# Performance work log

Hardware: AMD Instinct MI355X
Metric: run time of the kernel (lower is better)

The kernel has to match this reference:

```python
import jax, jax.numpy as jnp
import numpy as np

B, T, M = 32, 1024, 40
CD, H, C = 128, 256, 10  # conv_dims, rnn_hidden_dims, num_classes
DN = ('NCHW', 'OIHW', 'NCHW')


def _conv_block(x, W, b, pool):
    # 3x3 'same' conv + ReLU + max-pool (1, pool) over the mel axis
    y = jax.lax.conv_general_dilated(x, W, (1, 1), 'SAME', dimension_numbers=DN)
    y = jax.nn.relu(y + b[None, :, None, None])
    return jax.lax.reduce_window(y, -jnp.inf, jax.lax.max,
                                 (1, 1, 1, pool), (1, 1, 1, pool), 'VALID')


def setup_inputs() -> dict:
    key = jax.random.key(0)
    ks = jax.random.split(key, 12)
    inp = {}
    inp['x'] = jax.random.normal(ks[0], (B, 1, T, M), dtype=jnp.float32)
    inp['targets'] = (jax.random.uniform(ks[1], (B, T, C)) > 0.5).astype(jnp.float32)
    inp['force_mask'] = jax.random.randint(ks[2], (T, B), 0, 2, dtype=jnp.int32)
    s = 0.05
    inp['W1'] = jax.random.normal(ks[3], (CD, 1, 3, 3), dtype=jnp.float32) * s
    inp['b1'] = jnp.zeros((CD,), jnp.float32)
    inp['W2'] = jax.random.normal(ks[4], (CD, CD, 3, 3), dtype=jnp.float32) * s
    inp['b2'] = jnp.zeros((CD,), jnp.float32)
    inp['W3'] = jax.random.normal(ks[5], (CD, CD, 3, 3), dtype=jnp.float32) * s
    inp['b3'] = jnp.zeros((CD,), jnp.float32)
    inp['W_ih'] = jax.random.normal(ks[6], (3 * H, CD + C), dtype=jnp.float32) * s
    inp['W_hh'] = jax.random.normal(ks[7], (3 * H, H), dtype=jnp.float32) * s
    inp['b_ih'] = jnp.zeros((3 * H,), jnp.float32)
    inp['b_hh'] = jnp.zeros((3 * H,), jnp.float32)
    inp['Wf'] = jax.random.normal(ks[8], (C, H), dtype=jnp.float32) * s
    inp['bf'] = jnp.zeros((C,), jnp.float32)
    return inp


def reference(x, targets, force_mask, W1, b1, W2, b2, W3, b3,
              W_ih, W_hh, b_ih, b_hh, Wf, bf):
    # CNN feature extractor: mel axis 40 -> 8 -> 2 -> 1
    f = _conv_block(x, W1, b1, 5)
    f = _conv_block(f, W2, b2, 4)
    f = _conv_block(f, W3, b3, 2)          # [B, CD, T, 1]
    feats = f[..., 0].transpose(2, 0, 1)    # [T, B, CD]
    tgt_t = targets.transpose(1, 0, 2)       # [T, B, C]

    def step(carry, inp_t):
        h, tf = carry
        xt, tg, fm = inp_t                  # [B,CD], [B,C], [B]
        xc = jnp.concatenate([xt, tf], axis=-1)
        gi = xc @ W_ih.T + b_ih
        gh = h @ W_hh.T + b_hh
        i_r, i_z, i_n = jnp.split(gi, 3, axis=-1)
        h_r, h_z, h_n = jnp.split(gh, 3, axis=-1)
        r = jax.nn.sigmoid(i_r + h_r)
        z = jax.nn.sigmoid(i_z + h_z)
        n = jnp.tanh(i_n + r * h_n)
        h_new = (1.0 - z) * n + z * h
        out = h_new @ Wf.T + bf             # [B, C]
        pred = (jax.nn.sigmoid(out) > 0.5).astype(out.dtype)
        tf_new = jnp.where(fm[:, None] > 0, tg, pred)
        return (h_new, tf_new), out

    h0 = jnp.zeros((B, H), x.dtype)
    tf0 = jnp.zeros((B, C), x.dtype)
    _, outs = jax.lax.scan(step, (h0, tf0), (feats, tgt_t, force_mask))
    return outs.transpose(1, 0, 2)          # [B, T, C]
```

## Files before the change

kernel.cpp:

```cpp
#include <hip/hip_runtime.h>
#include <math.h>

#define B_ 32
#define T_ 1024
#define M_ 40

__global__ void prep_kernel(const float* __restrict__ W_hh, const float* __restrict__ W2,
                            const float* __restrict__ W3, const float* __restrict__ W_ih,
                            float* __restrict__ WhhT, float* __restrict__ W2t,
                            float* __restrict__ W3t, float* __restrict__ WihT4) {
  int idx = blockIdx.x * 256 + threadIdx.x;
  if (idx < 196608) {
    int k = idx / 768, j = idx % 768;
    WhhT[idx] = W_hh[j * 256 + k];
    return;
  }
  idx -= 196608;
  if (idx < 147456) {
    int tap = idx >> 14, ci = (idx >> 7) & 127, co = idx & 127;
    W2t[idx] = W2[(co * 128 + ci) * 9 + tap];
    return;
  }
  idx -= 147456;
  if (idx < 147456) {
    int tap = idx >> 14, ci = (idx >> 7) & 127, co = idx & 127;
    W3t[idx] = W3[(co * 128 + ci) * 9 + tap];
    return;
  }
  idx -= 147456;
  if (idx < 98304) {
    int khi = idx / 3072, rem = idx % 3072, j = rem >> 2, klo = rem & 3;
    WihT4[idx] = W_ih[j * 138 + khi * 4 + klo];
  }
}

__global__ __launch_bounds__(256) void conv12_kernel(
    const float* __restrict__ x, const float* __restrict__ W1, const float* __restrict__ b1,
    const float* __restrict__ W2t, const float* __restrict__ b2, float* __restrict__ y2) {
  __shared__ float xt[8 * 42];
  __shared__ float y1s[6 * 128 * 12];
  const int tid = threadIdx.x;
  const int t0 = blockIdx.x * 4;
  const int b = blockIdx.y;
  for (int idx = tid; idx < 8 * 42; idx += 256) {
    int row = idx / 42, slot = idx % 42;
    int t_in = t0 - 2 + row, m = slot - 1;
    float v = 0.f;
    if (t_in >= 0 && t_in < T_ && m >= 0 && m < M_) v = x[(b * T_ + t_in) * M_ + m];
    xt[idx] = v;
  }
  __syncthreads();
  const int c = tid & 127, q = tid >> 7;
  float w1[9];
#pragma unroll
  for (int i = 0; i < 9; ++i) w1[i] = W1[c * 9 + i];
  const float b1c = b1[c];
  for (int rr = 0; rr < 3; ++rr) {
    const int r = q * 3 + rr;
    const int t_in = t0 - 1 + r;
    float* yrow = &y1s[(r * 128 + c) * 12];
    if (t_in < 0 || t_in >= T_) {
#pragma unroll
      for (int s = 0; s < 12; ++s) yrow[s] = 0.f;
    } else {
      yrow[0] = 0.f; yrow[9] = 0.f; yrow[10] = 0.f; yrow[11] = 0.f;
#pragma unroll
      for (int mo = 0; mo < 8; ++mo) {
        float mx = -1e30f;
#pragma unroll
        for (int i5 = 0; i5 < 5; ++i5) {
          const int mp = mo * 5 + i5;
          float s = b1c;
#pragma unroll
          for (int dt = 0; dt < 3; ++dt)
#pragma unroll
            for (int dm = 0; dm < 3; ++dm)
              s += xt[(r + dt) * 42 + mp + dm] * w1[dt * 3 + dm];
          mx = fmaxf(mx, s);
        }
        yrow[1 + mo] = fmaxf(mx, 0.f);
      }
    }
  }
  __syncthreads();
  const int co = c, tq = q;
  float acc[2][8];
#pragma unroll
  for (int tl = 0; tl < 2; ++tl)
#pragma unroll
    for (int mo = 0; mo < 8; ++mo) acc[tl][mo] = 0.f;
  for (int ci = 0; ci < 128; ++ci) {
    float w[9];
#pragma unroll
    for (int i = 0; i < 9; ++i) w[i] = W2t[i * 16384 + ci * 128 + co];
    float xv[4][10];
#pragma unroll
    for (int rr = 0; rr < 4; ++rr) {
      const float* p = &y1s[((2 * tq + rr) * 128 + ci) * 12];
      const float4 a = *(const float4*)p;
      const float4 bq = *(const float4*)(p + 4);
      const float2 cq = *(const float2*)(p + 8);
      xv[rr][0] = a.x; xv[rr][1] = a.y; xv[rr][2] = a.z; xv[rr][3] = a.w;
      xv[rr][4] = bq.x; xv[rr][5] = bq.y; xv[rr][6] = bq.z; xv[rr][7] = bq.w;
      xv[rr][8] = cq.x; xv[rr][9] = cq.y;
    }
#pragma unroll
    for (int dt = 0; dt < 3; ++dt)
#pragma unroll
      for (int dm = 0; dm < 3; ++dm) {
        const float wv = w[dt * 3 + dm];
#pragma unroll
        for (int tl = 0; tl < 2; ++tl)
#pragma unroll
          for (int mo = 0; mo < 8; ++mo)
            acc[tl][mo] += xv[tl + dt][mo + dm] * wv;
      }
  }
  const float b2c = b2[co];
#pragma unroll
  for (int tl = 0; tl < 2; ++tl) {
    const int t = t0 + 2 * tq + tl;
    float m0 = fmaxf(fmaxf(acc[tl][0], acc[tl][1]), fmaxf(acc[tl][2], acc[tl][3])) + b2c;
    float m1 = fmaxf(fmaxf(acc[tl][4], acc[tl][5]), fmaxf(acc[tl][6], acc[tl][7])) + b2c;
    y2[((b * T_ + t) * 2 + 0) * 128 + co] = fmaxf(m0, 0.f);
    y2[((b * T_ + t) * 2 + 1) * 128 + co] = fmaxf(m1, 0.f);
  }
}

__global__ __launch_bounds__(256) void conv3_kernel(
    const float* __restrict__ y2, const float* __restrict__ W3t, const float* __restrict__ b3,
    float* __restrict__ feats) {
  __shared__ float y2s[6 * 128 * 4];
  const int tid = threadIdx.x;
  const int t0 = blockIdx.x * 4;
  const int b = blockIdx.y;
  for (int idx = tid; idx < 768; idx += 256) {
    int row = idx / 128, ci = idx % 128;
    y2s[(row * 128 + ci) * 4 + 0] = 0.f;
    y2s[(row * 128 + ci) * 4 + 3] = 0.f;
  }
  for (int idx = tid; idx < 6 * 256; idx += 256) {
    int row = idx / 256, rem = idx % 256;
    int m = rem >> 7, ci = rem & 127;
    int t_in = t0 - 1 + row;
    float v = 0.f;
    if (t_in >= 0 && t_in < T_) v = y2[((b * T_ + t_in) * 2 + m) * 128 + ci];
    y2s[(row * 128 + ci) * 4 + 1 + m] = v;
  }
  __syncthreads();
  const int co = tid & 127, tq = tid >> 7;
  float acc[2][2] = {{0.f, 0.f}, {0.f, 0.f}};
  for (int ci = 0; ci < 128; ++ci) {
    float w[9];
#pragma unroll
    for (int i = 0; i < 9; ++i) w[i] = W3t[i * 16384 + ci * 128 + co];
    float4 xr[4];
#pragma unroll
    for (int rr = 0; rr < 4; ++rr)
      xr[rr] = *(const float4*)&y2s[((2 * tq + rr) * 128 + ci) * 4];
#pragma unroll
    for (int dt = 0; dt < 3; ++dt)
#pragma unroll
      for (int tl = 0; tl < 2; ++tl) {
        const float4 v = xr[tl + dt];
        acc[tl][0] += v.y * w[dt * 3 + 1] + v.z * w[dt * 3 + 2];
        acc[tl][1] += v.y * w[dt * 3 + 0] + v.z * w[dt * 3 + 1];
      }
  }
  const float b3c = b3[co];
#pragma unroll
  for (int tl = 0; tl < 2; ++tl) {
    const int t = t0 + 2 * tq + tl;
    float f = fmaxf(fmaxf(acc[tl][0], acc[tl][1]) + b3c, 0.f);
    feats[(t * B_ + b) * 128 + co] = f;
  }
}

__global__ __launch_bounds__(256) void gid_kernel(
    const float* __restrict__ feats, const float* __restrict__ WihT4,
    const float* __restrict__ b_ih, float* __restrict__ gi) {
  __shared__ float fs[32 * 128];
  const int tid = threadIdx.x;
  const int jb = blockIdx.x;
  const int rb = blockIdx.y;
  const float4* src = (const float4*)(feats + rb * 32 * 128);
  float4* dst = (float4*)fs;
  for (int i = tid; i < 1024; i += 256) dst[i] = src[i];
  __syncthreads();
  const int j = jb * 256 + tid;
  float acc[32];
#pragma unroll
  for (int r = 0; r < 32; ++r) acc[r] = 0.f;
  for (int k4 = 0; k4 < 32; ++k4) {
    const float4 w4 = *(const float4*)&WihT4[(k4 * 768 + j) * 4];
#pragma unroll
    for (int r = 0; r < 32; ++r) {
      const float4 f4 = *(const float4*)&fs[r * 128 + k4 * 4];
      acc[r] += f4.x * w4.x + f4.y * w4.y + f4.z * w4.z + f4.w * w4.w;
    }
  }
  const float bj = b_ih[j];
  for (int r = 0; r < 32; ++r) gi[(rb * 32 + r) * 768 + j] = acc[r] + bj;
}

__global__ __launch_bounds__(768, 3) void rnn_kernel(
    const float* __restrict__ gi, const float* __restrict__ WhhT,
    const float* __restrict__ W_ih, const float* __restrict__ b_hh,
    const float* __restrict__ Wf, const float* __restrict__ bf,
    const float* __restrict__ targets, const int* __restrict__ force_mask,
    float* __restrict__ out) {
  __shared__ float Wl[2 * 8 * 1536];
  __shared__ float h_s[256];
  __shared__ float tf_s[16];
  __shared__ float gis[768];
  __shared__ float part[4 * 768];
  __shared__ float wtf[10 * 768];
  __shared__ float wfs[10 * 256];
  __shared__ float bhh_s[768];
  __shared__ float bf_s[16];
  const int tid = threadIdx.x;
  const int b = blockIdx.x;
  for (int idx = tid; idx < 7680; idx += 768) {
    int cc = idx / 768, j = idx % 768;
    wtf[idx] = W_ih[j * 138 + 128 + cc];
  }
  for (int idx = tid; idx < 2560; idx += 768) wfs[idx] = Wf[idx];
  bhh_s[tid] = b_hh[tid];
  if (tid < 256) h_s[tid] = 0.f;
  if (tid < 10) { tf_s[tid] = 0.f; bf_s[tid] = bf[tid]; }
  const int ks = tid / 192;
  const int jq = tid % 192;
  const float* wbase = WhhT + (ks * 64) * 768 + jq * 4;
  float4 wr[6][4];
#pragma unroll
  for (int g = 0; g < 6; ++g) {
    const float* wp0 = wbase + g * 3072;
    wr[g][0] = *(const float4*)(wp0);
    wr[g][1] = *(const float4*)(wp0 + 768);
    wr[g][2] = *(const float4*)(wp0 + 1536);
    wr[g][3] = *(const float4*)(wp0 + 2304);
  }
#pragma unroll
  for (int gg = 0; gg < 2; ++gg) {
    const float* src = wbase + (6 + gg) * 3072;
#pragma unroll
    for (int fp = 0; fp < 8; ++fp) {
      const int f0 = 2 * fp, f1 = 2 * fp + 1;
      Wl[(gg * 8 + fp) * 1536 + tid * 2 + 0] = src[(f0 >> 2) * 768 + (f0 & 3)];
      Wl[(gg * 8 + fp) * 1536 + tid * 2 + 1] = src[(f1 >> 2) * 768 + (f1 & 3)];
    }
  }
  __syncthreads();

  auto matvec = [&](int tt) {
    float giv = gi[(tt * B_ + b) * 768 + tid];
    float4 a4 = make_float4(0.f, 0.f, 0.f, 0.f);
#pragma unroll
    for (int g = 0; g < 6; ++g) {
      const float4 h4 = *(const float4*)&h_s[ks * 64 + g * 4];
      a4.x += wr[g][0].x * h4.x + wr[g][1].x * h4.y + wr[g][2].x * h4.z + wr[g][3].x * h4.w;
      a4.y += wr[g][0].y * h4.x + wr[g][1].y * h4.y + wr[g][2].y * h4.z + wr[g][3].y * h4.w;
      a4.z += wr[g][0].z * h4.x + wr[g][1].z * h4.y + wr[g][2].z * h4.z + wr[g][3].z * h4.w;
      a4.w += wr[g][0].w * h4.x + wr[g][1].w * h4.y + wr[g][2].w * h4.z + wr[g][3].w * h4.w;
    }
#pragma unroll
    for (int gg = 0; gg < 2; ++gg) {
      const float4 h4 = *(const float4*)&h_s[ks * 64 + (6 + gg) * 4];
      const float* base = &Wl[(gg * 8) * 1536 + tid * 2];
      const float2 p0 = *(const float2*)(base);
      const float2 p1 = *(const float2*)(base + 1536);
      const float2 p2 = *(const float2*)(base + 3072);
      const float2 p3 = *(const float2*)(base + 4608);
      const float2 p4 = *(const float2*)(base + 6144);
      const float2 p5 = *(const float2*)(base + 7680);
      const float2 p6 = *(const float2*)(base + 9216);
      const float2 p7 = *(const float2*)(base + 10752);
      a4.x += p0.x * h4.x + p2.x * h4.y + p4.x * h4.z + p6.x * h4.w;
      a4.y += p0.y * h4.x + p2.y * h4.y + p4.y * h4.z + p6.y * h4.w;
      a4.z += p1.x * h4.x + p3.x * h4.y + p5.x * h4.z + p7.x * h4.w;
      a4.w += p1.y * h4.x + p3.y * h4.y + p5.y * h4.z + p7.y * h4.w;
    }
    const float* wp = wbase + 8 * 3072;
#pragma unroll 2
    for (int g8 = 8; g8 < 16; ++g8) {
      const float4 w0 = *(const float4*)(wp);
      const float4 w1v = *(const float4*)(wp + 768);
      const float4 w2v = *(const float4*)(wp + 1536);
      const float4 w3v = *(const float4*)(wp + 2304);
      const float4 h4 = *(const float4*)&h_s[ks * 64 + g8 * 4];
      a4.x += w0.x * h4.x + w1v.x * h4.y + w2v.x * h4.z + w3v.x * h4.w;
      a4.y += w0.y * h4.x + w1v.y * h4.y + w2v.y * h4.z + w3v.y * h4.w;
      a4.z += w0.z * h4.x + w1v.z * h4.y + w2v.z * h4.z + w3v.z * h4.w;
      a4.w += w0.w * h4.x + w1v.w * h4.y + w2v.w * h4.z + w3v.w * h4.w;
      wp += 3072;
    }
    *(float4*)&part[ks * 768 + jq * 4] = a4;
    gis[tid] = giv;
  };

  int fm_r = 0;
  float tg_r[10];
  if (tid == 0) {
    fm_r = force_mask[0 * B_ + b];
#pragma unroll
    for (int cc = 0; cc < 10; ++cc) tg_r[cc] = targets[(b * T_ + 0) * 10 + cc];
  }
  matvec(0);
  __syncthreads();

  for (int t = 0; t < T_; ++t) {
    if (tid < 256) {
      const int j = tid;
      float gr = gis[j], gz = gis[256 + j], gn0 = gis[512 + j];
#pragma unroll
      for (int cc = 0; cc < 10; ++cc) {
        const float tfv = tf_s[cc];
        gr += wtf[cc * 768 + j] * tfv;
        gz += wtf[cc * 768 + 256 + j] * tfv;
        gn0 += wtf[cc * 768 + 512 + j] * tfv;
      }
      float ghr = bhh_s[j] + part[j] + part[768 + j] + part[1536 + j] + part[2304 + j];
      float ghz = bhh_s[256 + j] + part[256 + j] + part[1024 + j] + part[1792 + j] + part[2560 + j];
      float ghn = bhh_s[512 + j] + part[512 + j] + part[1280 + j] + part[2048 + j] + part[2816 + j];
      const float r = 1.f / (1.f + expf(-(gr + ghr)));
      const float z = 1.f / (1.f + expf(-(gz + ghz)));
      const float n = tanhf(gn0 + r * ghn);
      h_s[j] = (1.f - z) * n + z * h_s[j];
    }
    __syncthreads();
    if (tid < 64) {
      const float h0 = h_s[tid], h1 = h_s[tid + 64], h2 = h_s[tid + 128], h3 = h_s[tid + 192];
      float p[10];
#pragma unroll
      for (int cc = 0; cc < 10; ++cc)
        p[cc] = wfs[cc * 256 + tid] * h0 + wfs[cc * 256 + tid + 64] * h1 +
                wfs[cc * 256 + tid + 128] * h2 + wfs[cc * 256 + tid + 192] * h3;
#pragma unroll
      for (int off = 32; off > 0; off >>= 1)
#pragma unroll
        for (int cc = 0; cc < 10; ++cc) p[cc] += __shfl_xor(p[cc], off);
      if (tid == 0) {
#pragma unroll
        for (int cc = 0; cc < 10; ++cc) {
          const float o = p[cc] + bf_s[cc];
          out[(b * T_ + t) * 10 + cc] = o;
          tf_s[cc] = (fm_r > 0) ? tg_r[cc] : (o > 0.f ? 1.f : 0.f);
        }
        if (t + 1 < T_) {
          fm_r = force_mask[(t + 1) * B_ + b];
#pragma unroll
          for (int cc = 0; cc < 10; ++cc) tg_r[cc] = targets[(b * T_ + t + 1) * 10 + cc];
        }
      }
    }
    if (t + 1 < T_) matvec(t + 1);
    __syncthreads();
  }
}

extern "C" void kernel_launch(void* const* d_in, const int* in_sizes, int n_in,
                              void* d_out, int out_size, void* d_ws, size_t ws_size,
                              hipStream_t stream) {
  const float* x = (const float*)d_in[0];
  const float* targets = (const float*)d_in[1];
  const int* fmask = (const int*)d_in[2];
  const float* W1 = (const float*)d_in[3];
  const float* b1 = (const float*)d_in[4];
  const float* W2 = (const float*)d_in[5];
  const float* b2 = (const float*)d_in[6];
  const float* W3 = (const float*)d_in[7];
  const float* b3 = (const float*)d_in[8];
  const float* Wih = (const float*)d_in[9];
  const float* Whh = (const float*)d_in[10];
  const float* bih = (const float*)d_in[11];
  const float* bhh = (const float*)d_in[12];
  const float* Wf = (const float*)d_in[13];
  const float* bf = (const float*)d_in[14];
  float* out = (float*)d_out;
  float* ws = (float*)d_ws;
  float* WhhT = ws;
  float* W2t = ws + 196608;
  float* W3t = ws + 344064;
  float* WihT4 = ws + 491520;
  float* feats = ws + 589824;
  float* gi = ws + 4784128;
  float* y2 = gi;

  prep_kernel<<<2304, 256, 0, stream>>>(Whh, W2, W3, Wih, WhhT, W2t, W3t, WihT4);
  conv12_kernel<<<dim3(256, 32), 256, 0, stream>>>(x, W1, b1, W2t, b2, y2);
  conv3_kernel<<<dim3(256, 32), 256, 0, stream>>>(y2, W3t, b3, feats);
  gid_kernel<<<dim3(3, 1024), 256, 0, stream>>>(feats, WihT4, bih, gi);
  rnn_kernel<<<32, 768, 0, stream>>>(gi, WhhT, Wih, bhh, Wf, bf, targets, fmask, out);
}
```

Measured before the change: 7.228 ms.

## Split GRU recurrence across 8 blocks per batch with global flag sync

The recurrent kernel previously ran one 768-thread block per batch row, doing the full 256x768 hidden matvec each step. Now each batch row is split across 8 blocks, each holding a 32-column slice of W_hh (all three gates) in shared memory. The blocks exchange hidden state through a double-buffered global buffer and synchronise with per-slice release/acquire flags. This spreads the serial matvec over more compute units, but adds a global-memory round trip and a spin-wait on every timestep. The output projection is computed one step late and redundantly in every slice.

After: 12.28 ms. 1.7x slower.

```diff
diff --git a/kernel.cpp b/kernel.cpp
--- a/kernel.cpp
+++ b/kernel.cpp
@@ -203,158 +203,177 @@
   for (int r = 0; r < 32; ++r) gi[(rb * 32 + r) * 768 + j] = acc[r] + bj;
 }
 
-__global__ __launch_bounds__(768, 3) void rnn_kernel(
+__global__ void zflags_kernel(int* __restrict__ flags) { flags[threadIdx.x] = 0; }
+
+__global__ __launch_bounds__(256) void rnn_kernel(
     const float* __restrict__ gi, const float* __restrict__ WhhT,
     const float* __restrict__ W_ih, const float* __restrict__ b_hh,
     const float* __restrict__ Wf, const float* __restrict__ bf,
     const float* __restrict__ targets, const int* __restrict__ force_mask,
-    float* __restrict__ out) {
-  __shared__ float Wl[2 * 8 * 1536];
-  __shared__ float h_s[256];
-  __shared__ float tf_s[16];
-  __shared__ float gis[768];
-  __shared__ float part[4 * 768];
-  __shared__ float wtf[10 * 768];
-  __shared__ float wfs[10 * 256];
-  __shared__ float bhh_s[768];
-  __shared__ float bf_s[16];
+    float* __restrict__ out, float* __restrict__ Hbuf, int* __restrict__ flags) {
+  __shared__ float4 Wsl4[6144];
+  __shared__ float4 part4[96];
+  __shared__ __align__(16) float h_s[256];
+  __shared__ float wtf_l[960];
+  __shared__ float wfs[2560];
+  __shared__ float bhh_l[96];
+  __shared__ float tf_s[10];
+  __shared__ float bf_s[10];
+  float* Wslf = (float*)Wsl4;
+  float* partf = (float*)part4;
   const int tid = threadIdx.x;
-  const int b = blockIdx.x;
-  for (int idx = tid; idx < 7680; idx += 768) {
-    int cc = idx / 768, j = idx % 768;
-    wtf[idx] = W_ih[j * 138 + 128 + cc];
-  }
-  for (int idx = tid; idx < 2560; idx += 768) wfs[idx] = Wf[idx];
-  bhh_s[tid] = b_hh[tid];
-  if (tid < 256) h_s[tid] = 0.f;
+  const int batch = blockIdx.x & 31;
+  const int slice = blockIdx.x >> 5;
+#pragma unroll 4
+  for (int idx = tid; idx < 24576; idx += 256) {
+    const int k = idx / 96, lr = idx % 96;
+    const int jg = (lr >> 5) * 256 + slice * 32 + (lr & 31);
+    Wslf[idx] = WhhT[k * 768 + jg];
+  }
+  for (int idx = tid; idx < 960; idx += 256) {
+    const int cc = idx / 96, lr = idx % 96;
+    const int jg = (lr >> 5) * 256 + slice * 32 + (lr & 31);
+    wtf_l[idx] = W_ih[jg * 138 + 128 + cc];
+  }
+  for (int idx = tid; idx < 2560; idx += 256) wfs[idx] = Wf[idx];
+  if (tid < 96) {
+    const int jg = (tid >> 5) * 256 + slice * 32 + (tid & 31);
+    bhh_l[tid] = b_hh[jg];
+  }
+  h_s[tid] = 0.f;
   if (tid < 10) { tf_s[tid] = 0.f; bf_s[tid] = bf[tid]; }
-  const int ks = tid / 192;
-  const int jq = tid % 192;
-  const float* wbase = WhhT + (ks * 64) * 768 + jq * 4;
-  float4 wr[6][4];
-#pragma unroll
-  for (int g = 0; g < 6; ++g) {
-    const float* wp0 = wbase + g * 3072;
-    wr[g][0] = *(const float4*)(wp0);
-    wr[g][1] = *(const float4*)(wp0 + 768);
-    wr[g][2] = *(const float4*)(wp0 + 1536);
-    wr[g][3] = *(const float4*)(wp0 + 2304);
-  }
-#pragma unroll
-  for (int gg = 0; gg < 2; ++gg) {
-    const float* src = wbase + (6 + gg) * 3072;
-#pragma unroll
-    for (int fp = 0; fp < 8; ++fp) {
-      const int f0 = 2 * fp, f1 = 2 * fp + 1;
-      Wl[(gg * 8 + fp) * 1536 + tid * 2 + 0] = src[(f0 >> 2) * 768 + (f0 & 3)];
-      Wl[(gg * 8 + fp) * 1536 + tid * 2 + 1] = src[(f1 >> 2) * 768 + (f1 & 3)];
-    }
-  }
-  __syncthreads();
-
-  auto matvec = [&](int tt) {
-    float giv = gi[(tt * B_ + b) * 768 + tid];
-    float4 a4 = make_float4(0.f, 0.f, 0.f, 0.f);
-#pragma unroll
-    for (int g = 0; g < 6; ++g) {
-      const float4 h4 = *(const float4*)&h_s[ks * 64 + g * 4];
-      a4.x += wr[g][0].x * h4.x + wr[g][1].x * h4.y + wr[g][2].x * h4.z + wr[g][3].x * h4.w;
-      a4.y += wr[g][0].y * h4.x + wr[g][1].y * h4.y + wr[g][2].y * h4.z + wr[g][3].y * h4.w;
-      a4.z += wr[g][0].z * h4.x + wr[g][1].z * h4.y + wr[g][2].z * h4.z + wr[g][3].z * h4.w;
-      a4.w += wr[g][0].w * h4.x + wr[g][1].w * h4.y + wr[g][2].w * h4.z + wr[g][3].w * h4.w;
-    }
-#pragma unroll
-    for (int gg = 0; gg < 2; ++gg) {
-      const float4 h4 = *(const float4*)&h_s[ks * 64 + (6 + gg) * 4];
-      const float* base = &Wl[(gg * 8) * 1536 + tid * 2];
-      const float2 p0 = *(const float2*)(base);
-      const float2 p1 = *(const float2*)(base + 1536);
-      const float2 p2 = *(const float2*)(base + 3072);
-      const float2 p3 = *(const float2*)(base + 4608);
-      const float2 p4 = *(const float2*)(base + 6144);
-      const float2 p5 = *(const float2*)(base + 7680);
-      const float2 p6 = *(const float2*)(base + 9216);
-      const float2 p7 = *(const float2*)(base + 10752);
-      a4.x += p0.x * h4.x + p2.x * h4.y + p4.x * h4.z + p6.x * h4.w;
-      a4.y += p0.y * h4.x + p2.y * h4.y + p4.y * h4.z + p6.y * h4.w;
-      a4.z += p1.x * h4.x + p3.x * h4.y + p5.x * h4.z + p7.x * h4.w;
-      a4.w += p1.y * h4.x + p3.y * h4.y + p5.y * h4.z + p7.y * h4.w;
-    }
-    const float* wp = wbase + 8 * 3072;
-#pragma unroll 2
-    for (int g8 = 8; g8 < 16; ++g8) {
-      const float4 w0 = *(const float4*)(wp);
-      const float4 w1v = *(const float4*)(wp + 768);
-      const float4 w2v = *(const float4*)(wp + 1536);
-      const float4 w3v = *(const float4*)(wp + 2304);
-      const float4 h4 = *(const float4*)&h_s[ks * 64 + g8 * 4];
-      a4.x += w0.x * h4.x + w1v.x * h4.y + w2v.x * h4.z + w3v.x * h4.w;
-      a4.y += w0.y * h4.x + w1v.y * h4.y + w2v.y * h4.z + w3v.y * h4.w;
-      a4.z += w0.z * h4.x + w1v.z * h4.y + w2v.z * h4.z + w3v.z * h4.w;
-      a4.w += w0.w * h4.x + w1v.w * h4.y + w2v.w * h4.z + w3v.w * h4.w;
-      wp += 3072;
-    }
-    *(float4*)&part[ks * 768 + jq * 4] = a4;
-    gis[tid] = giv;
-  };
-
   int fm_r = 0;
   float tg_r[10];
   if (tid == 0) {
-    fm_r = force_mask[0 * B_ + b];
-#pragma unroll
-    for (int cc = 0; cc < 10; ++cc) tg_r[cc] = targets[(b * T_ + 0) * 10 + cc];
-  }
-  matvec(0);
-  __syncthreads();
+    fm_r = force_mask[batch];
+#pragma unroll
+    for (int cc = 0; cc < 10; ++cc) tg_r[cc] = targets[(batch * T_) * 10 + cc];
+  }
+  __syncthreads();
+
+  const int mt = tid - 64;
+  const bool mv = (mt >= 0 && mt < 96);
+  const int q = mv ? mt % 24 : 0;
+  const int ks = mv ? mt / 24 : 0;
+  int* const bflags = flags + batch * 8;
+  int* const myflag = bflags + slice;
 
   for (int t = 0; t < T_; ++t) {
-    if (tid < 256) {
-      const int j = tid;
-      float gr = gis[j], gz = gis[256 + j], gn0 = gis[512 + j];
+    if (t > 0) {
+      if (tid < 8) {
+        while (__hip_atomic_load(bflags + tid, __ATOMIC_ACQUIRE,
+                                 __HIP_MEMORY_SCOPE_AGENT) < t)
+          __builtin_amdgcn_s_sleep(1);
+      }
+      __syncthreads();
+      if (tid < 64) {
+        const float* hb = Hbuf + ((t - 1) & 1) * 8192 + batch * 256;
+#pragma unroll
+        for (int u = 0; u < 4; ++u)
+          h_s[tid * 4 + u] = __hip_atomic_load(hb + tid * 4 + u, __ATOMIC_RELAXED,
+                                               __HIP_MEMORY_SCOPE_AGENT);
+      }
+      __syncthreads();
+    }
+    float gi_r = 0.f, gi_z = 0.f, gi_n = 0.f;
+    if (tid < 32) {
+      const int gb = (t * B_ + batch) * 768 + slice * 32 + tid;
+      gi_r = gi[gb]; gi_z = gi[gb + 256]; gi_n = gi[gb + 512];
+    }
+    if (mv) {
+      const float4* wp = Wsl4 + ks * 1536 + q;
+      float4 a4 = make_float4(0.f, 0.f, 0.f, 0.f);
+#pragma unroll
+      for (int g = 0; g < 16; ++g) {
+        const float4 h4 = *(const float4*)&h_s[ks * 64 + g * 4];
+        const float4 w0 = wp[g * 96];
+        const float4 w1 = wp[g * 96 + 24];
+        const float4 w2 = wp[g * 96 + 48];
+        const float4 w3 = wp[g * 96 + 72];
+        a4.x += w0.x * h4.x + w1.x * h4.y + w2.x * h4.z + w3.x * h4.w;
+        a4.y += w0.y * h4.x + w1.y * h4.y + w2.y * h4.z + w3.y * h4.w;
+        a4.z += w0.z * h4.x + w1.z * h4.y + w2.z * h4.z + w3.z * h4.w;
+        a4.w += w0.w * h4.x + w1.w * h4.y + w2.w * h4.z + w3.w * h4.w;
+      }
+      part4[ks * 24 + q] = a4;
+    }
+    if (t > 0 && tid < 64) {
+      const float h0 = h_s[tid], h1 = h_s[tid + 64], h2 = h_s[tid + 128], h3 = h_s[tid + 192];
+      float p[10];
+#pragma unroll
+      for (int cc = 0; cc < 10; ++cc)
+        p[cc] = wfs[cc * 256 + tid] * h0 + wfs[cc * 256 + tid + 64] * h1 +
+                wfs[cc * 256 + tid + 128] * h2 + wfs[cc * 256 + tid + 192] * h3;
+#pragma unroll
+      for (int off = 32; off > 0; off >>= 1)
+#pragma unroll
+        for (int cc = 0; cc < 10; ++cc) p[cc] += __shfl_xor(p[cc], off);
+      if (tid == 0) {
+#pragma unroll
+        for (int cc = 0; cc < 10; ++cc) {
+          const float o = p[cc] + bf_s[cc];
+          if (slice == 0) out[(batch * T_ + (t - 1)) * 10 + cc] = o;
+          tf_s[cc] = (fm_r > 0) ? tg_r[cc] : (o > 0.f ? 1.f : 0.f);
+        }
+        fm_r = force_mask[t * B_ + batch];
+#pragma unroll
+        for (int cc = 0; cc < 10; ++cc) tg_r[cc] = targets[(batch * T_ + t) * 10 + cc];
+      }
+    }
+    __syncthreads();
+    if (tid < 32) {
+      const int d = tid;
+      float gr = gi_r, gz = gi_z, gn0 = gi_n;
 #pragma unroll
       for (int cc = 0; cc < 10; ++cc) {
         const float tfv = tf_s[cc];
-        gr += wtf[cc * 768 + j] * tfv;
-        gz += wtf[cc * 768 + 256 + j] * tfv;
-        gn0 += wtf[cc * 768 + 512 + j] * tfv;
-      }
-      float ghr = bhh_s[j] + part[j] + part[768 + j] + part[1536 + j] + part[2304 + j];
-      float ghz = bhh_s[256 + j] + part[256 + j] + part[1024 + j] + part[1792 + j] + part[2560 + j];
-      float ghn = bhh_s[512 + j] + part[512 + j] + part[1280 + j] + part[2048 + j] + part[2816 + j];
+        gr += wtf_l[cc * 96 + d] * tfv;
+        gz += wtf_l[cc * 96 + 32 + d] * tfv;
+        gn0 += wtf_l[cc * 96 + 64 + d] * tfv;
+      }
+      const float ghr = bhh_l[d] + partf[d] + partf[96 + d] + partf[192 + d] + partf[288 + d];
+      const float ghz = bhh_l[32 + d] + partf[32 + d] + partf[128 + d] + partf[224 + d] + partf[320 + d];
+      const float ghn = bhh_l[64 + d] + partf[64 + d] + partf[160 + d] + partf[256 + d] + partf[352 + d];
       const float r = 1.f / (1.f + expf(-(gr + ghr)));
       const float z = 1.f / (1.f + expf(-(gz + ghz)));
       const float n = tanhf(gn0 + r * ghn);
-      h_s[j] = (1.f - z) * n + z * h_s[j];
-    }
-    __syncthreads();
-    if (tid < 64) {
-      const float h0 = h_s[tid], h1 = h_s[tid + 64], h2 = h_s[tid + 128], h3 = h_s[tid + 192];
-      float p[10];
+      const float hn = (1.f - z) * n + z * h_s[slice * 32 + d];
+      __hip_atomic_store(Hbuf + (t & 1) * 8192 + batch * 256 + slice * 32 + d, hn,
+                         __ATOMIC_RELAXED, __HIP_MEMORY_SCOPE_AGENT);
+      __threadfence();
+      if (d == 0)
+        __hip_atomic_store(myflag, t + 1, __ATOMIC_RELEASE, __HIP_MEMORY_SCOPE_AGENT);
+    }
+  }
+  if (tid < 8) {
+    while (__hip_atomic_load(bflags + tid, __ATOMIC_ACQUIRE, __HIP_MEMORY_SCOPE_AGENT) < T_)
+      __builtin_amdgcn_s_sleep(1);
+  }
+  __syncthreads();
+  if (tid < 64) {
+    const float* hb = Hbuf + ((T_ - 1) & 1) * 8192 + batch * 256;
+#pragma unroll
+    for (int u = 0; u < 4; ++u)
+      h_s[tid * 4 + u] = __hip_atomic_load(hb + tid * 4 + u, __ATOMIC_RELAXED,
+                                           __HIP_MEMORY_SCOPE_AGENT);
+  }
+  __syncthreads();
+  if (slice == 0 && tid < 64) {
+    const float h0 = h_s[tid], h1 = h_s[tid + 64], h2 = h_s[tid + 128], h3 = h_s[tid + 192];
+    float p[10];
+#pragma unroll
+    for (int cc = 0; cc < 10; ++cc)
+      p[cc] = wfs[cc * 256 + tid] * h0 + wfs[cc * 256 + tid + 64] * h1 +
+              wfs[cc * 256 + tid + 128] * h2 + wfs[cc * 256 + tid + 192] * h3;
+#pragma unroll
+    for (int off = 32; off > 0; off >>= 1)
+#pragma unroll
+      for (int cc = 0; cc < 10; ++cc) p[cc] += __shfl_xor(p[cc], off);
+    if (tid == 0) {
 #pragma unroll
       for (int cc = 0; cc < 10; ++cc)
-        p[cc] = wfs[cc * 256 + tid] * h0 + wfs[cc * 256 + tid + 64] * h1 +
-                wfs[cc * 256 + tid + 128] * h2 + wfs[cc * 256 + tid + 192] * h3;
-#pragma unroll
-      for (int off = 32; off > 0; off >>= 1)
-#pragma unroll
-        for (int cc = 0; cc < 10; ++cc) p[cc] += __shfl_xor(p[cc], off);
-      if (tid == 0) {
-#pragma unroll
-        for (int cc = 0; cc < 10; ++cc) {
-          const float o = p[cc] + bf_s[cc];
-          out[(b * T_ + t) * 10 + cc] = o;
-          tf_s[cc] = (fm_r > 0) ? tg_r[cc] : (o > 0.f ? 1.f : 0.f);
-        }
-        if (t + 1 < T_) {
-          fm_r = force_mask[(t + 1) * B_ + b];
-#pragma unroll
-          for (int cc = 0; cc < 10; ++cc) tg_r[cc] = targets[(b * T_ + t + 1) * 10 + cc];
-        }
-      }
-    }
-    if (t + 1 < T_) matvec(t + 1);
-    __syncthreads();
+        out[(batch * T_ + (T_ - 1)) * 10 + cc] = p[cc] + bf_s[cc];
+    }
   }
 }
 
@@ -385,10 +404,14 @@
   float* feats = ws + 589824;
   float* gi = ws + 4784128;
   float* y2 = gi;
+  float* Hbuf = feats;
+  int* flags = (int*)(feats + 16384);
 
   prep_kernel<<<2304, 256, 0, stream>>>(Whh, W2, W3, Wih, WhhT, W2t, W3t, WihT4);
   conv12_kernel<<<dim3(256, 32), 256, 0, stream>>>(x, W1, b1, W2t, b2, y2);
   conv3_kernel<<<dim3(256, 32), 256, 0, stream>>>(y2, W3t, b3, feats);
   gid_kernel<<<dim3(3, 1024), 256, 0, stream>>>(feats, WihT4, bih, gi);
-  rnn_kernel<<<32, 768, 0, stream>>>(gi, WhhT, Wih, bhh, Wf, bf, targets, fmask, out);
-}
+  zflags_kernel<<<1, 256, 0, stream>>>(flags);
+  rnn_kernel<<<256, 256, 0, stream>>>(gi, WhhT, Wih, bhh, Wf, bf, targets, fmask,
+                                      out, Hbuf, flags);
+}
```
